# Kernel optimization log

Hardware: AMD Instinct MI355X
Metric: run time of the kernel (lower is better)

## Reference

```python
import jax, jax.numpy as jnp
import numpy as np

ALPHA, BETA, GAMMA = 1.0, 1.0, 0.001
DELTA_V, DELTA_D = 0.5, 1.5
NORM = 2


def _lp_norm(x, p, axis):
    # grad-safe Lp norm: avoids d/dx sqrt(0) NaNs on exactly-zero rows (diagonal pairs)
    ss = jnp.sum(jnp.abs(x) ** p, axis=axis)
    safe = jnp.where(ss > 0, ss, 1.0)
    return jnp.where(ss > 0, safe ** (1.0 / p), 0.0)


def setup_inputs() -> dict:
    key = jax.random.key(0)
    k1, k2, k3 = jax.random.split(key, 3)
    bs, n_filters, H, W, n_inst = 8, 16, 128, 128, 24
    inp = jax.random.normal(k1, (bs, n_filters, H, W), dtype=jnp.float32)
    target = jax.random.randint(k2, (bs, n_inst, H, W), 0, 2).astype(jnp.int32)
    # every sample has at least 2 objects so dist term is exercised and no 0/0
    n_objects = jax.random.randint(k3, (bs, 1), 2, n_inst + 1).astype(jnp.int32)
    return {"input": inp, "target": target, "n_objects": n_objects, "max_n_objects": n_inst}


def reference(input, target, n_objects, max_n_objects):
    bs, n_filters, H, W = input.shape
    n_inst = target.shape[1]
    L = H * W
    pred = jnp.transpose(input, (0, 2, 3, 1)).reshape(bs, L, n_filters)  # (bs, L, F)
    gt = jnp.transpose(target, (0, 2, 3, 1)).reshape(bs, L, n_inst).astype(jnp.float32)  # (bs, L, I)

    nobj = n_objects[:, 0]  # (bs,)
    nf = nobj.astype(jnp.float32)
    valid = (jnp.arange(n_inst)[None, :] < nobj[:, None]).astype(jnp.float32)  # (bs, I)
    gt_m = gt * valid[:, None, :]

    # cluster means: masked sum / masked count, zero-filled past n_objects
    counts = gt_m.sum(axis=1)  # (bs, I)
    sums = jnp.einsum('bli,blf->bif', gt_m, pred)  # (bs, I, F)
    means = jnp.where((valid > 0)[..., None],
                      sums / jnp.where(counts > 0, counts, 1.0)[..., None], 0.0)

    # variance term
    dn = _lp_norm(pred[:, :, None, :] - means[:, None, :, :], NORM, 3)  # (bs, L, I)
    var = jnp.maximum(dn - DELTA_V, 0.0) ** 2 * gt
    var_num = jnp.sum(var * valid[:, None, :], axis=(1, 2))
    var_den = jnp.sum(gt_m, axis=(1, 2))
    var_term = jnp.mean(var_num / var_den)

    # distance term (pairwise hinge over valid instance pairs)
    mdn = _lp_norm(means[:, :, None, :] - means[:, None, :, :], NORM, 3)  # (bs, I, I)
    margin = 2.0 * DELTA_D * (1.0 - jnp.eye(n_inst, dtype=jnp.float32))[None]
    pair_mask = valid[:, :, None] * valid[:, None, :]
    hinge = jnp.maximum(margin - mdn, 0.0) ** 2 * pair_mask
    denom = jnp.where(nf > 1, nf * (nf - 1.0), 1.0)
    per_sample = jnp.where(nf > 1, jnp.sum(hinge, axis=(1, 2)) / denom, 0.0)
    dist_term = jnp.mean(per_sample)

    # regularization term
    row_norms = _lp_norm(means, NORM, 2)  # (bs, I)
    reg_term = jnp.mean(jnp.sum(row_norms * valid, axis=1) / nf)

    return ALPHA * var_term + BETA * dist_term + GAMMA * reg_term
```

## Files before the change

kernel.cpp:

```cpp
#include <hip/hip_runtime.h>

#define BS 8
#define NF 16
#define NI 24
#define LL 16384

#define OFF_COUNTS 0
#define OFF_SUMS   192
#define OFF_MEANS  3264
#define OFF_VDEN   6336
#define OFF_DIST   6344
#define OFF_REG    6352
#define OFF_VNUM   6360
#define WS_FLOATS  6368

#define TL 128
#define CHUNKS_A 32
#define VBLK 32

__device__ __forceinline__ float block_sum(float v, volatile float* red) {
    for (int off = 32; off; off >>= 1) v += __shfl_down(v, off);
    __syncthreads();
    if ((threadIdx.x & 63) == 0) red[threadIdx.x >> 6] = v;
    __syncthreads();
    float r = 0.f;
    int nw = blockDim.x >> 6;
    if ((int)threadIdx.x < nw) r = red[threadIdx.x];
    if ((threadIdx.x >> 6) == 0)
        for (int off = 32; off; off >>= 1) r += __shfl_down(r, off);
    return r;
}

__global__ __launch_bounds__(384) void k_sums(const float* __restrict__ input,
                                              const int* __restrict__ target,
                                              float* __restrict__ ws) {
    __shared__ float pred_lds[TL][NF + 1];
    __shared__ float tgt_lds[NI][TL];
    const int b = blockIdx.y;
    const int t = threadIdx.x;
    const int i = t >> 4;
    const int f = t & 15;
    const float* inb = input + (size_t)b * NF * LL;
    const int*   tgb = target + (size_t)b * NI * LL;

    float acc = 0.f, cnt = 0.f;
    const int l0base = blockIdx.x * (LL / CHUNKS_A);
    for (int tile = 0; tile < (LL / CHUNKS_A) / TL; ++tile) {
        const int l0 = l0base + tile * TL;
        for (int idx = t; idx < NF * TL; idx += 384) {
            int ff = idx >> 7;
            int j  = idx & (TL - 1);
            pred_lds[j][ff] = inb[ff * LL + l0 + j];
        }
        for (int idx = t; idx < NI * TL; idx += 384) {
            int ii = idx >> 7;
            int j  = idx & (TL - 1);
            tgt_lds[ii][j] = (float)tgb[ii * LL + l0 + j];
        }
        __syncthreads();
        #pragma unroll 8
        for (int j = 0; j < TL; ++j) {
            float tv = tgt_lds[i][j];
            acc = fmaf(tv, pred_lds[j][f], acc);
            if (f == 0) cnt += tv;
        }
        __syncthreads();
    }
    atomicAdd(&ws[OFF_SUMS + (b * NI + i) * NF + f], acc);
    if (f == 0) atomicAdd(&ws[OFF_COUNTS + b * NI + i], cnt);
}

__global__ __launch_bounds__(256) void k_means_dist_reg(const int* __restrict__ n_objects,
                                                        float* __restrict__ ws) {
    const int b = blockIdx.x;
    const int t = threadIdx.x;
    const int n = n_objects[b];
    __shared__ float m_lds[NI][NF];
    __shared__ float red[8];

    for (int idx = t; idx < NI * NF; idx += 256) {
        int i = idx >> 4, f = idx & 15;
        float c = ws[OFF_COUNTS + b * NI + i];
        float s = ws[OFF_SUMS + (b * NI + i) * NF + f];
        float m = (i < n) ? s / (c > 0.f ? c : 1.f) : 0.f;
        m_lds[i][f] = m;
        ws[OFF_MEANS + (b * NI + i) * NF + f] = m;
    }
    __syncthreads();

    float vden = 0.f, reg = 0.f;
    if (t < NI && t < n) {
        vden = ws[OFF_COUNTS + b * NI + t];
        float ss = 0.f;
        #pragma unroll
        for (int f = 0; f < NF; ++f) { float m = m_lds[t][f]; ss += m * m; }
        reg = (ss > 0.f) ? sqrtf(ss) : 0.f;
    }
    float dist = 0.f;
    for (int p = t; p < NI * NI; p += 256) {
        int i = p / NI, j = p % NI;
        if (i != j && i < n && j < n) {
            float ss = 0.f;
            #pragma unroll
            for (int f = 0; f < NF; ++f) { float d = m_lds[i][f] - m_lds[j][f]; ss += d * d; }
            float dn = (ss > 0.f) ? sqrtf(ss) : 0.f;
            float h = fmaxf(3.0f - dn, 0.f);
            dist += h * h;
        }
    }
    float vden_s = block_sum(vden, red);
    float reg_s  = block_sum(reg, red);
    float dist_s = block_sum(dist, red);
    if (t == 0) {
        ws[OFF_VDEN + b] = vden_s;
        ws[OFF_REG + b]  = reg_s / (float)n;
        float nf = (float)n;
        ws[OFF_DIST + b] = (n > 1) ? dist_s / (nf * (nf - 1.f)) : 0.f;
    }
}

__global__ __launch_bounds__(256) void k_var(const float* __restrict__ input,
                                             const int* __restrict__ target,
                                             const int* __restrict__ n_objects,
                                             float* __restrict__ ws) {
    const int b = blockIdx.y;
    const int n = n_objects[b];
    const int t = threadIdx.x;
    __shared__ float m_lds[NI][NF];
    __shared__ float red[8];
    for (int idx = t; idx < NI * NF; idx += 256)
        m_lds[idx >> 4][idx & 15] = ws[OFF_MEANS + b * NI * NF + idx];
    __syncthreads();

    const float* inb = input + (size_t)b * NF * LL;
    const int*   tgb = target + (size_t)b * NI * LL;
    float acc = 0.f;
    for (int l = blockIdx.x * 256 + t; l < LL; l += VBLK * 256) {
        float p[NF];
        #pragma unroll
        for (int f = 0; f < NF; ++f) p[f] = inb[f * LL + l];
        for (int i = 0; i < n; ++i) {
            float tv = (float)tgb[i * LL + l];
            float ss = 0.f;
            #pragma unroll
            for (int f = 0; f < NF; ++f) { float d = p[f] - m_lds[i][f]; ss = fmaf(d, d, ss); }
            float dn = (ss > 0.f) ? sqrtf(ss) : 0.f;
            float h = fmaxf(dn - 0.5f, 0.f);
            acc = fmaf(tv, h * h, acc);
        }
    }
    float s = block_sum(acc, red);
    if (t == 0) atomicAdd(&ws[OFF_VNUM + b], s);
}

__global__ void k_final(const float* __restrict__ ws, float* __restrict__ out) {
    if (threadIdx.x == 0 && blockIdx.x == 0) {
        float vt = 0.f, dt = 0.f, rt = 0.f;
        for (int b = 0; b < BS; ++b) {
            vt += ws[OFF_VNUM + b] / ws[OFF_VDEN + b];
            dt += ws[OFF_DIST + b];
            rt += ws[OFF_REG + b];
        }
        out[0] = (1.0f * vt + 1.0f * dt + 0.001f * rt) * (1.0f / (float)BS);
    }
}

extern "C" void kernel_launch(void* const* d_in, const int* in_sizes, int n_in,
                              void* d_out, int out_size, void* d_ws, size_t ws_size,
                              hipStream_t stream) {
    const float* input     = (const float*)d_in[0];
    const int*   target    = (const int*)d_in[1];
    const int*   n_objects = (const int*)d_in[2];
    float* ws  = (float*)d_ws;
    float* out = (float*)d_out;

    hipMemsetAsync(d_ws, 0, WS_FLOATS * sizeof(float), stream);

    dim3 gA(CHUNKS_A, BS);
    k_sums<<<gA, 384, 0, stream>>>(input, target, ws);
    k_means_dist_reg<<<BS, 256, 0, stream>>>(n_objects, ws);
    dim3 gC(VBLK, BS);
    k_var<<<gC, 256, 0, stream>>>(input, target, n_objects, ws);
    k_final<<<1, 64, 0, stream>>>(ws, out);
}
```

Before: 107.6 us.

## Register-tile cluster sums per wavefront and vectorize variance loads with float4

k_sums drops its LDS tiling. Each wavefront now owns three instances and accumulates all 16 features in registers over float4/int4 loads, then reduces with shuffles before the atomics. k_var now has each thread handle four contiguous pixels with float4 loads and no grid-stride loop, using 16 blocks per sample. The aim is to remove LDS traffic and syncs and to widen global loads. The cost is much higher register pressure (48 accumulators plus 64 prediction values), which may lower occupancy. Each wavefront in k_sums also reloads the prediction data for its own instances.

```diff
diff --git a/kernel.cpp b/kernel.cpp
--- a/kernel.cpp
+++ b/kernel.cpp
@@ -14,9 +14,9 @@
 #define OFF_VNUM   6360
 #define WS_FLOATS  6368
 
-#define TL 128
-#define CHUNKS_A 32
-#define VBLK 32
+#define L_CHUNKS 32
+#define I_PER 3
+#define VBLK 16
 
 __device__ __forceinline__ float block_sum(float v, volatile float* red) {
     for (int off = 32; off; off >>= 1) v += __shfl_down(v, off);
@@ -31,43 +31,68 @@
     return r;
 }
 
-__global__ __launch_bounds__(384) void k_sums(const float* __restrict__ input,
+__global__ __launch_bounds__(512) void k_sums(const float* __restrict__ input,
                                               const int* __restrict__ target,
                                               float* __restrict__ ws) {
-    __shared__ float pred_lds[TL][NF + 1];
-    __shared__ float tgt_lds[NI][TL];
-    const int b = blockIdx.y;
-    const int t = threadIdx.x;
-    const int i = t >> 4;
-    const int f = t & 15;
+    const int b    = blockIdx.y;
+    const int w    = threadIdx.x >> 6;
+    const int lane = threadIdx.x & 63;
+    const int i0   = w * I_PER;
+    const int l0   = blockIdx.x * (LL / L_CHUNKS);
     const float* inb = input + (size_t)b * NF * LL;
     const int*   tgb = target + (size_t)b * NI * LL;
 
-    float acc = 0.f, cnt = 0.f;
-    const int l0base = blockIdx.x * (LL / CHUNKS_A);
-    for (int tile = 0; tile < (LL / CHUNKS_A) / TL; ++tile) {
-        const int l0 = l0base + tile * TL;
-        for (int idx = t; idx < NF * TL; idx += 384) {
-            int ff = idx >> 7;
-            int j  = idx & (TL - 1);
-            pred_lds[j][ff] = inb[ff * LL + l0 + j];
-        }
-        for (int idx = t; idx < NI * TL; idx += 384) {
-            int ii = idx >> 7;
-            int j  = idx & (TL - 1);
-            tgt_lds[ii][j] = (float)tgb[ii * LL + l0 + j];
-        }
-        __syncthreads();
-        #pragma unroll 8
-        for (int j = 0; j < TL; ++j) {
-            float tv = tgt_lds[i][j];
-            acc = fmaf(tv, pred_lds[j][f], acc);
-            if (f == 0) cnt += tv;
-        }
-        __syncthreads();
-    }
-    atomicAdd(&ws[OFF_SUMS + (b * NI + i) * NF + f], acc);
-    if (f == 0) atomicAdd(&ws[OFF_COUNTS + b * NI + i], cnt);
+    float acc[I_PER][NF];
+    float cnt[I_PER];
+    #pragma unroll
+    for (int ii = 0; ii < I_PER; ++ii) {
+        cnt[ii] = 0.f;
+        #pragma unroll
+        for (int f = 0; f < NF; ++f) acc[ii][f] = 0.f;
+    }
+
+    #pragma unroll
+    for (int step = 0; step < (LL / L_CHUNKS) / 256; ++step) {
+        const int l = l0 + step * 256 + lane * 4;
+        float4 p[NF];
+        #pragma unroll
+        for (int f = 0; f < NF; ++f)
+            p[f] = *reinterpret_cast<const float4*>(inb + f * LL + l);
+        #pragma unroll
+        for (int ii = 0; ii < I_PER; ++ii) {
+            int4 tv = *reinterpret_cast<const int4*>(tgb + (i0 + ii) * LL + l);
+            float t0 = (float)tv.x, t1 = (float)tv.y, t2 = (float)tv.z, t3 = (float)tv.w;
+            cnt[ii] += (t0 + t1) + (t2 + t3);
+            #pragma unroll
+            for (int f = 0; f < NF; ++f) {
+                float a = acc[ii][f];
+                a = fmaf(t0, p[f].x, a);
+                a = fmaf(t1, p[f].y, a);
+                a = fmaf(t2, p[f].z, a);
+                a = fmaf(t3, p[f].w, a);
+                acc[ii][f] = a;
+            }
+        }
+    }
+
+    #pragma unroll
+    for (int ii = 0; ii < I_PER; ++ii) {
+        #pragma unroll
+        for (int f = 0; f < NF; ++f)
+            for (int off = 32; off; off >>= 1)
+                acc[ii][f] += __shfl_down(acc[ii][f], off);
+        for (int off = 32; off; off >>= 1)
+            cnt[ii] += __shfl_down(cnt[ii], off);
+    }
+    if (lane == 0) {
+        #pragma unroll
+        for (int ii = 0; ii < I_PER; ++ii) {
+            #pragma unroll
+            for (int f = 0; f < NF; ++f)
+                atomicAdd(&ws[OFF_SUMS + (b * NI + i0 + ii) * NF + f], acc[ii][f]);
+            atomicAdd(&ws[OFF_COUNTS + b * NI + i0 + ii], cnt[ii]);
+        }
+    }
 }
 
 __global__ __launch_bounds__(256) void k_means_dist_reg(const int* __restrict__ n_objects,
@@ -134,20 +159,32 @@
 
     const float* inb = input + (size_t)b * NF * LL;
     const int*   tgb = target + (size_t)b * NI * LL;
+    const int l = (blockIdx.x * 256 + t) * 4;
+
+    float4 p[NF];
+    #pragma unroll
+    for (int f = 0; f < NF; ++f)
+        p[f] = *reinterpret_cast<const float4*>(inb + f * LL + l);
+
     float acc = 0.f;
-    for (int l = blockIdx.x * 256 + t; l < LL; l += VBLK * 256) {
-        float p[NF];
-        #pragma unroll
-        for (int f = 0; f < NF; ++f) p[f] = inb[f * LL + l];
-        for (int i = 0; i < n; ++i) {
-            float tv = (float)tgb[i * LL + l];
-            float ss = 0.f;
-            #pragma unroll
-            for (int f = 0; f < NF; ++f) { float d = p[f] - m_lds[i][f]; ss = fmaf(d, d, ss); }
-            float dn = (ss > 0.f) ? sqrtf(ss) : 0.f;
-            float h = fmaxf(dn - 0.5f, 0.f);
-            acc = fmaf(tv, h * h, acc);
-        }
+    for (int i = 0; i < n; ++i) {
+        int4 tv = *reinterpret_cast<const int4*>(tgb + i * LL + l);
+        float s0 = 0.f, s1 = 0.f, s2 = 0.f, s3 = 0.f;
+        #pragma unroll
+        for (int f = 0; f < NF; ++f) {
+            float m = m_lds[i][f];
+            float d0 = p[f].x - m, d1 = p[f].y - m, d2 = p[f].z - m, d3 = p[f].w - m;
+            s0 = fmaf(d0, d0, s0); s1 = fmaf(d1, d1, s1);
+            s2 = fmaf(d2, d2, s2); s3 = fmaf(d3, d3, s3);
+        }
+        float h0 = fmaxf(sqrtf(s0) - 0.5f, 0.f);
+        float h1 = fmaxf(sqrtf(s1) - 0.5f, 0.f);
+        float h2 = fmaxf(sqrtf(s2) - 0.5f, 0.f);
+        float h3 = fmaxf(sqrtf(s3) - 0.5f, 0.f);
+        acc = fmaf((float)tv.x, h0 * h0, acc);
+        acc = fmaf((float)tv.y, h1 * h1, acc);
+        acc = fmaf((float)tv.z, h2 * h2, acc);
+        acc = fmaf((float)tv.w, h3 * h3, acc);
     }
     float s = block_sum(acc, red);
     if (t == 0) atomicAdd(&ws[OFF_VNUM + b], s);
@@ -176,8 +213,8 @@
 
     hipMemsetAsync(d_ws, 0, WS_FLOATS * sizeof(float), stream);
 
-    dim3 gA(CHUNKS_A, BS);
-    k_sums<<<gA, 384, 0, stream>>>(input, target, ws);
+    dim3 gA(L_CHUNKS, BS);
+    k_sums<<<gA, 512, 0, stream>>>(input, target, ws);
     k_means_dist_reg<<<BS, 256, 0, stream>>>(n_objects, ws);
     dim3 gC(VBLK, BS);
     k_var<<<gC, 256, 0, stream>>>(input, target, n_objects, ws);
```

Result: slower. 122.4 us (+13.7%).
